# Kernel tuning notes

Measured on AMD Instinct MI355X. Metric: run time of the kernel, lower is better.

Reference implementation:

```python
import jax, jax.numpy as jnp
import numpy as np

B, T, RNN_DIM, ENC_DIM, ATT_DIM, NFILT, KSIZE = 256, 1024, 1024, 512, 128, 32, 31
PAD = (KSIZE - 1) // 2


def setup_inputs() -> dict:
    key = jax.random.key(0)
    ks = jax.random.split(key, 10)
    attn = jax.random.uniform(ks[3], (B, T), dtype=jnp.float32)
    attn = attn / jnp.sum(attn, axis=1, keepdims=True)  # previous-step alignment (sums to 1)
    return {
        "query": jax.random.normal(ks[0], (B, RNN_DIM), dtype=jnp.float32),
        "memory": jax.random.normal(ks[1], (B, T, ENC_DIM), dtype=jnp.float32),
        "processed_memory": jax.random.normal(ks[2], (B, T, ATT_DIM), dtype=jnp.float32),
        "attn_weights": attn,
        "attn_weights_cum": jax.random.uniform(ks[4], (B, T), dtype=jnp.float32),
        "memory_lengths": jax.random.randint(ks[5], (B,), T // 2, T + 1),
        "conv_w": jax.random.normal(ks[6], (NFILT, 2, KSIZE), dtype=jnp.float32) * 0.1,
        "W_loc": jax.random.normal(ks[7], (ATT_DIM, NFILT), dtype=jnp.float32) * 0.1,
        "W_q": jax.random.normal(ks[8], (ATT_DIM, RNN_DIM), dtype=jnp.float32) * 0.03,
        "v_w": jax.random.normal(ks[9], (1, ATT_DIM), dtype=jnp.float32) * 0.1,
        "v_b": jnp.zeros((1,), dtype=jnp.float32),
    }


def reference(query, memory, processed_memory, attn_weights, attn_weights_cum,
              memory_lengths, conv_w, W_loc, W_q, v_w, v_b):
    Tlen = memory.shape[1]
    # [B, 2, T]: stack prev + cumulative alignments
    cat = jnp.stack([attn_weights, attn_weights_cum], axis=1)
    # location conv: Conv1d(2 -> NFILT, k=31, same padding, no bias) -> [B, NFILT, T]
    loc = jax.lax.conv_general_dilated(
        cat, conv_w, window_strides=(1,), padding=[(PAD, PAD)],
        dimension_numbers=("NCH", "OIH", "NCH"))
    # location_dense: [B, T, ATT_DIM]
    processed_location = jnp.einsum("bct,ac->bta", loc, W_loc)
    # query projection: [B, 1, ATT_DIM]
    processed_query = (query @ W_q.T)[:, None, :]
    # additive energies: v . tanh(q + loc + mem) -> [B, T]
    hidden = jnp.tanh(processed_query + processed_location + processed_memory)
    energies = jnp.einsum("bta,a->bt", hidden, v_w[0]) + v_b[0]
    # mask padded positions (pos >= length) with -inf
    mask = jnp.arange(Tlen)[None, :] >= memory_lengths[:, None]
    energies = jnp.where(mask, -jnp.inf, energies)
    new_attn = jax.nn.softmax(energies, axis=1)
    new_cum = attn_weights_cum + new_attn
    # context: [B, ENC_DIM]
    context = jnp.einsum("bt,bte->be", new_attn, memory)
    return context, new_attn, new_cum
```

## Files before the change

kernel.cpp:

```cpp
#include <hip/hip_runtime.h>
#include <math.h>

#define Bc 256
#define Tc 1024
#define RNN_DIMc 1024
#define ENC_DIMc 512
#define ATT_DIMc 128
#define NFILTc 32
#define KSIZEc 31
#define PADc 15

__device__ __forceinline__ float fast_tanh(float x) {
    x = fminf(15.f, fmaxf(-15.f, x));
    float z = __expf(2.f * x);
    return (z - 1.f) / (z + 1.f);
}

__device__ __forceinline__ float wave_reduce_max(float x) {
#pragma unroll
    for (int off = 32; off > 0; off >>= 1) x = fmaxf(x, __shfl_xor(x, off, 64));
    return x;
}

__device__ __forceinline__ float wave_reduce_sum(float x) {
#pragma unroll
    for (int off = 32; off > 0; off >>= 1) x += __shfl_xor(x, off, 64);
    return x;
}

__global__ __launch_bounds__(128) void qproj_k(const float* __restrict__ query,
                                               const float* __restrict__ W_q,
                                               float* __restrict__ pq) {
    const int b = blockIdx.x;
    __shared__ float q[RNN_DIMc];
    for (int i = threadIdx.x; i < RNN_DIMc; i += 128) q[i] = query[b * RNN_DIMc + i];
    __syncthreads();
    const float* w = W_q + (size_t)threadIdx.x * RNN_DIMc;
    float acc = 0.f;
#pragma unroll 4
    for (int r = 0; r < RNN_DIMc; r += 4) {
        float4 wv = *(const float4*)(w + r);
        acc = fmaf(wv.x, q[r + 0], acc);
        acc = fmaf(wv.y, q[r + 1], acc);
        acc = fmaf(wv.z, q[r + 2], acc);
        acc = fmaf(wv.w, q[r + 3], acc);
    }
    pq[b * ATT_DIMc + threadIdx.x] = acc;
}

__global__ __launch_bounds__(256) void energies_k(
    const float* __restrict__ attn_w, const float* __restrict__ cum_w,
    const float* __restrict__ pm, const float* __restrict__ pq,
    const float* __restrict__ conv_w, const float* __restrict__ W_loc,
    const float* __restrict__ v_w, const float* __restrict__ v_b,
    const int* __restrict__ lens, float* __restrict__ energies) {
    const int b = blockIdx.x >> 2;
    const int t0 = (blockIdx.x & 3) * 256;
    const int t = t0 + threadIdx.x;

    __shared__ float s_a[256 + 2 * PADc];
    __shared__ float s_c[256 + 2 * PADc];
    for (int i = threadIdx.x; i < 256 + 2 * PADc; i += 256) {
        int tt = t0 - PADc + i;
        bool ok = (tt >= 0) && (tt < Tc);
        s_a[i] = ok ? attn_w[b * Tc + tt] : 0.f;
        s_c[i] = ok ? cum_w[b * Tc + tt] : 0.f;
    }
    __syncthreads();

    float wa[KSIZEc], wcm[KSIZEc];
#pragma unroll
    for (int k = 0; k < KSIZEc; ++k) {
        wa[k] = s_a[threadIdx.x + k];
        wcm[k] = s_c[threadIdx.x + k];
    }

    float loc[NFILTc];
#pragma unroll
    for (int f = 0; f < NFILTc; ++f) {
        const float* cw = conv_w + f * (2 * KSIZEc);
        float a0 = 0.f, a1 = 0.f;
#pragma unroll
        for (int k = 0; k < KSIZEc; ++k) {
            a0 = fmaf(cw[k], wa[k], a0);
            a1 = fmaf(cw[KSIZEc + k], wcm[k], a1);
        }
        loc[f] = a0 + a1;
    }

    const float* pmrow = pm + ((size_t)(b * Tc + t)) * ATT_DIMc;
    const float* pqr = pq + b * ATT_DIMc;
    float e = 0.f;
#pragma unroll 2
    for (int a = 0; a < ATT_DIMc; a += 4) {
        float4 pmv = *(const float4*)(pmrow + a);
        const float* wl = W_loc + a * NFILTc;
        float pl0 = 0.f, pl1 = 0.f, pl2 = 0.f, pl3 = 0.f;
#pragma unroll
        for (int f = 0; f < NFILTc; ++f) {
            float lf = loc[f];
            pl0 = fmaf(wl[f], lf, pl0);
            pl1 = fmaf(wl[NFILTc + f], lf, pl1);
            pl2 = fmaf(wl[2 * NFILTc + f], lf, pl2);
            pl3 = fmaf(wl[3 * NFILTc + f], lf, pl3);
        }
        e = fmaf(v_w[a + 0], fast_tanh(pqr[a + 0] + pl0 + pmv.x), e);
        e = fmaf(v_w[a + 1], fast_tanh(pqr[a + 1] + pl1 + pmv.y), e);
        e = fmaf(v_w[a + 2], fast_tanh(pqr[a + 2] + pl2 + pmv.z), e);
        e = fmaf(v_w[a + 3], fast_tanh(pqr[a + 3] + pl3 + pmv.w), e);
    }
    e += v_b[0];
    if (t >= lens[b]) e = -INFINITY;
    energies[b * Tc + t] = e;
}

__global__ __launch_bounds__(256) void softmax_k(const float* __restrict__ energies,
                                                 const float* __restrict__ cum_in,
                                                 float* __restrict__ out_attn,
                                                 float* __restrict__ out_cum) {
    const int b = blockIdx.x;
    const float* e = energies + b * Tc;
    float ev[4];
    float m = -INFINITY;
#pragma unroll
    for (int i = 0; i < 4; ++i) {
        ev[i] = e[threadIdx.x + 256 * i];
        m = fmaxf(m, ev[i]);
    }
    m = wave_reduce_max(m);
    __shared__ float redm[4];
    __shared__ float reds[4];
    const int wid = threadIdx.x >> 6;
    if ((threadIdx.x & 63) == 0) redm[wid] = m;
    __syncthreads();
    m = fmaxf(fmaxf(redm[0], redm[1]), fmaxf(redm[2], redm[3]));

    float p[4];
    float s = 0.f;
#pragma unroll
    for (int i = 0; i < 4; ++i) {
        p[i] = __expf(ev[i] - m);
        s += p[i];
    }
    s = wave_reduce_sum(s);
    if ((threadIdx.x & 63) == 0) reds[wid] = s;
    __syncthreads();
    s = reds[0] + reds[1] + reds[2] + reds[3];
    float inv = 1.f / s;
#pragma unroll
    for (int i = 0; i < 4; ++i) {
        int t = threadIdx.x + 256 * i;
        float na = p[i] * inv;
        out_attn[b * Tc + t] = na;
        out_cum[b * Tc + t] = cum_in[b * Tc + t] + na;
    }
}

__global__ __launch_bounds__(512) void ctx_partial_k(const float* __restrict__ attn,
                                                     const float* __restrict__ memory,
                                                     float* __restrict__ partial) {
    const int b = blockIdx.x >> 2;
    const int seg = blockIdx.x & 3;
    const int e = threadIdx.x;
    const float* ar = attn + b * Tc + seg * 256;
    const float* mr = memory + ((size_t)(b * Tc + seg * 256)) * ENC_DIMc + e;
    float acc = 0.f;
#pragma unroll 4
    for (int tt = 0; tt < 256; ++tt) {
        acc = fmaf(ar[tt], mr[(size_t)tt * ENC_DIMc], acc);
    }
    partial[(size_t)blockIdx.x * ENC_DIMc + e] = acc;
}

__global__ __launch_bounds__(256) void ctx_reduce_k(const float* __restrict__ partial,
                                                    float* __restrict__ ctx) {
    const int idx = blockIdx.x * 256 + threadIdx.x;
    const int b = idx >> 9;
    const int e = idx & 511;
    float s = partial[(size_t)(b * 4 + 0) * ENC_DIMc + e] +
              partial[(size_t)(b * 4 + 1) * ENC_DIMc + e] +
              partial[(size_t)(b * 4 + 2) * ENC_DIMc + e] +
              partial[(size_t)(b * 4 + 3) * ENC_DIMc + e];
    ctx[idx] = s;
}

extern "C" void kernel_launch(void* const* d_in, const int* in_sizes, int n_in,
                              void* d_out, int out_size, void* d_ws, size_t ws_size,
                              hipStream_t stream) {
    const float* query  = (const float*)d_in[0];
    const float* memory = (const float*)d_in[1];
    const float* pm     = (const float*)d_in[2];
    const float* attn_w = (const float*)d_in[3];
    const float* cum_w  = (const float*)d_in[4];
    const int*   lens   = (const int*)d_in[5];
    const float* conv_w = (const float*)d_in[6];
    const float* W_loc  = (const float*)d_in[7];
    const float* W_q    = (const float*)d_in[8];
    const float* v_w    = (const float*)d_in[9];
    const float* v_b    = (const float*)d_in[10];

    float* out      = (float*)d_out;
    float* ctx      = out;
    float* out_attn = out + Bc * ENC_DIMc;
    float* out_cum  = out + Bc * ENC_DIMc + Bc * Tc;

    float* pq       = (float*)d_ws;
    float* energies = pq + Bc * ATT_DIMc;
    float* partial  = (float*)d_ws;

    qproj_k<<<Bc, 128, 0, stream>>>(query, W_q, pq);
    energies_k<<<Bc * 4, 256, 0, stream>>>(attn_w, cum_w, pm, pq, conv_w, W_loc, v_w, v_b,
                                           lens, energies);
    softmax_k<<<Bc, 256, 0, stream>>>(energies, cum_w, out_attn, out_cum);
    ctx_partial_k<<<Bc * 4, 512, 0, stream>>>(out_attn, memory, partial);
    ctx_reduce_k<<<(Bc * ENC_DIMc) / 256, 256, 0, stream>>>(partial, ctx);
}
```

Before: 861.2 us.

## Fuse all attention stages into one per-batch 1024-thread kernel

```diff
diff --git a/kernel.cpp b/kernel.cpp
--- a/kernel.cpp
+++ b/kernel.cpp
@@ -28,160 +28,144 @@
     return x;
 }
 
-__global__ __launch_bounds__(128) void qproj_k(const float* __restrict__ query,
-                                               const float* __restrict__ W_q,
-                                               float* __restrict__ pq) {
+__global__ __launch_bounds__(1024) void lsa_fused(
+    const float* __restrict__ query, const float* __restrict__ memory,
+    const float* __restrict__ pm, const float* __restrict__ attn_w,
+    const float* __restrict__ cum_w, const int* __restrict__ lens,
+    const float* __restrict__ conv_w, const float* __restrict__ W_loc,
+    const float* __restrict__ W_q, const float* __restrict__ v_w,
+    const float* __restrict__ v_b, float* __restrict__ ctx,
+    float* __restrict__ out_attn, float* __restrict__ out_cum) {
     const int b = blockIdx.x;
-    __shared__ float q[RNN_DIMc];
-    for (int i = threadIdx.x; i < RNN_DIMc; i += 128) q[i] = query[b * RNN_DIMc + i];
-    __syncthreads();
-    const float* w = W_q + (size_t)threadIdx.x * RNN_DIMc;
-    float acc = 0.f;
-#pragma unroll 4
-    for (int r = 0; r < RNN_DIMc; r += 4) {
-        float4 wv = *(const float4*)(w + r);
-        acc = fmaf(wv.x, q[r + 0], acc);
-        acc = fmaf(wv.y, q[r + 1], acc);
-        acc = fmaf(wv.z, q[r + 2], acc);
-        acc = fmaf(wv.w, q[r + 3], acc);
-    }
-    pq[b * ATT_DIMc + threadIdx.x] = acc;
-}
+    const int tid = threadIdx.x;
 
-__global__ __launch_bounds__(256) void energies_k(
-    const float* __restrict__ attn_w, const float* __restrict__ cum_w,
-    const float* __restrict__ pm, const float* __restrict__ pq,
-    const float* __restrict__ conv_w, const float* __restrict__ W_loc,
-    const float* __restrict__ v_w, const float* __restrict__ v_b,
-    const int* __restrict__ lens, float* __restrict__ energies) {
-    const int b = blockIdx.x >> 2;
-    const int t0 = (blockIdx.x & 3) * 256;
-    const int t = t0 + threadIdx.x;
+    __shared__ float s_q[RNN_DIMc];
+    __shared__ float s_pq[ATT_DIMc];
+    __shared__ float s_win0[Tc + 2 * PADc];
+    __shared__ float s_win1[Tc + 2 * PADc];
+    __shared__ float s_attn[Tc];
+    __shared__ float s_redm[16];
+    __shared__ float s_reds[16];
+    __shared__ float s_scratch[8][ENC_DIMc];
 
-    __shared__ float s_a[256 + 2 * PADc];
-    __shared__ float s_c[256 + 2 * PADc];
-    for (int i = threadIdx.x; i < 256 + 2 * PADc; i += 256) {
-        int tt = t0 - PADc + i;
+    if (tid < RNN_DIMc) s_q[tid] = query[b * RNN_DIMc + tid];
+    for (int i = tid; i < Tc + 2 * PADc; i += 1024) {
+        int tt = i - PADc;
         bool ok = (tt >= 0) && (tt < Tc);
-        s_a[i] = ok ? attn_w[b * Tc + tt] : 0.f;
-        s_c[i] = ok ? cum_w[b * Tc + tt] : 0.f;
+        s_win0[i] = ok ? attn_w[b * Tc + tt] : 0.f;
+        s_win1[i] = ok ? cum_w[b * Tc + tt] : 0.f;
     }
     __syncthreads();
 
-    float wa[KSIZEc], wcm[KSIZEc];
+    {
+        const int a = tid >> 3;
+        const int c = tid & 7;
+        const float* w = W_q + (size_t)a * RNN_DIMc + c * 128;
+        const float* qq = s_q + c * 128;
+        float acc = 0.f;
 #pragma unroll
-    for (int k = 0; k < KSIZEc; ++k) {
-        wa[k] = s_a[threadIdx.x + k];
-        wcm[k] = s_c[threadIdx.x + k];
+        for (int j = 0; j < 128; j += 4) {
+            float4 wv = *(const float4*)(w + j);
+            acc = fmaf(wv.x, qq[j + 0], acc);
+            acc = fmaf(wv.y, qq[j + 1], acc);
+            acc = fmaf(wv.z, qq[j + 2], acc);
+            acc = fmaf(wv.w, qq[j + 3], acc);
+        }
+        ((float*)s_scratch)[a * 8 + c] = acc;
+    }
+    __syncthreads();
+    if (tid < ATT_DIMc) {
+        const float* p = (const float*)s_scratch + tid * 8;
+        s_pq[tid] = p[0] + p[1] + p[2] + p[3] + p[4] + p[5] + p[6] + p[7];
+    }
+    __syncthreads();
+
+    const int t = tid;
+    float e;
+    {
+        float loc[NFILTc];
+#pragma unroll
+        for (int f = 0; f < NFILTc; ++f) loc[f] = 0.f;
+        for (int k = 0; k < KSIZEc; ++k) {
+            const float wa = s_win0[t + k];
+            const float wc = s_win1[t + k];
+#pragma unroll
+            for (int f = 0; f < NFILTc; ++f) {
+                loc[f] = fmaf(conv_w[f * (2 * KSIZEc) + k], wa, loc[f]);
+                loc[f] = fmaf(conv_w[f * (2 * KSIZEc) + KSIZEc + k], wc, loc[f]);
+            }
+        }
+
+        const float* pmrow = pm + ((size_t)(b * Tc + t)) * ATT_DIMc;
+        e = 0.f;
+#pragma unroll 2
+        for (int a = 0; a < ATT_DIMc; a += 4) {
+            float4 pmv = *(const float4*)(pmrow + a);
+            const float* wl = W_loc + a * NFILTc;
+            float pl0 = 0.f, pl1 = 0.f, pl2 = 0.f, pl3 = 0.f;
+#pragma unroll
+            for (int f = 0; f < NFILTc; ++f) {
+                float lf = loc[f];
+                pl0 = fmaf(wl[f], lf, pl0);
+                pl1 = fmaf(wl[NFILTc + f], lf, pl1);
+                pl2 = fmaf(wl[2 * NFILTc + f], lf, pl2);
+                pl3 = fmaf(wl[3 * NFILTc + f], lf, pl3);
+            }
+            e = fmaf(v_w[a + 0], fast_tanh(s_pq[a + 0] + pl0 + pmv.x), e);
+            e = fmaf(v_w[a + 1], fast_tanh(s_pq[a + 1] + pl1 + pmv.y), e);
+            e = fmaf(v_w[a + 2], fast_tanh(s_pq[a + 2] + pl2 + pmv.z), e);
+            e = fmaf(v_w[a + 3], fast_tanh(s_pq[a + 3] + pl3 + pmv.w), e);
+        }
+        e += v_b[0];
+        if (t >= lens[b]) e = -INFINITY;
     }
 
-    float loc[NFILTc];
+    {
+        float m = wave_reduce_max(e);
+        if ((tid & 63) == 0) s_redm[tid >> 6] = m;
+        __syncthreads();
+        float bm = s_redm[0];
 #pragma unroll
-    for (int f = 0; f < NFILTc; ++f) {
-        const float* cw = conv_w + f * (2 * KSIZEc);
-        float a0 = 0.f, a1 = 0.f;
+        for (int j = 1; j < 16; ++j) bm = fmaxf(bm, s_redm[j]);
+
+        float p = __expf(e - bm);
+        float s = wave_reduce_sum(p);
+        if ((tid & 63) == 0) s_reds[tid >> 6] = s;
+        __syncthreads();
+        float tot = 0.f;
 #pragma unroll
-        for (int k = 0; k < KSIZEc; ++k) {
-            a0 = fmaf(cw[k], wa[k], a0);
-            a1 = fmaf(cw[KSIZEc + k], wcm[k], a1);
+        for (int j = 0; j < 16; ++j) tot += s_reds[j];
+        float na = p * (1.f / tot);
+
+        out_attn[b * Tc + t] = na;
+        out_cum[b * Tc + t] = s_win1[t + PADc] + na;
+        s_attn[t] = na;
+    }
+    __syncthreads();
+
+    {
+        const int tr = tid >> 7;
+        const int e4 = (tid & 127) * 4;
+        const float* mb = memory + (size_t)b * Tc * ENC_DIMc;
+        float4 acc = make_float4(0.f, 0.f, 0.f, 0.f);
+#pragma unroll 4
+        for (int tt = tr; tt < Tc; tt += 8) {
+            const float w = s_attn[tt];
+            const float4 mv = *(const float4*)(mb + (size_t)tt * ENC_DIMc + e4);
+            acc.x = fmaf(w, mv.x, acc.x);
+            acc.y = fmaf(w, mv.y, acc.y);
+            acc.z = fmaf(w, mv.z, acc.z);
+            acc.w = fmaf(w, mv.w, acc.w);
         }
-        loc[f] = a0 + a1;
+        *(float4*)&s_scratch[tr][e4] = acc;
     }
-
-    const float* pmrow = pm + ((size_t)(b * Tc + t)) * ATT_DIMc;
-    const float* pqr = pq + b * ATT_DIMc;
-    float e = 0.f;
-#pragma unroll 2
-    for (int a = 0; a < ATT_DIMc; a += 4) {
-        float4 pmv = *(const float4*)(pmrow + a);
-        const float* wl = W_loc + a * NFILTc;
-        float pl0 = 0.f, pl1 = 0.f, pl2 = 0.f, pl3 = 0.f;
+    __syncthreads();
+    if (tid < ENC_DIMc) {
+        float s = 0.f;
 #pragma unroll
-        for (int f = 0; f < NFILTc; ++f) {
-            float lf = loc[f];
-            pl0 = fmaf(wl[f], lf, pl0);
-            pl1 = fmaf(wl[NFILTc + f], lf, pl1);
-            pl2 = fmaf(wl[2 * NFILTc + f], lf, pl2);
-            pl3 = fmaf(wl[3 * NFILTc + f], lf, pl3);
-        }
-        e = fmaf(v_w[a + 0], fast_tanh(pqr[a + 0] + pl0 + pmv.x), e);
-        e = fmaf(v_w[a + 1], fast_tanh(pqr[a + 1] + pl1 + pmv.y), e);
-        e = fmaf(v_w[a + 2], fast_tanh(pqr[a + 2] + pl2 + pmv.z), e);
-        e = fmaf(v_w[a + 3], fast_tanh(pqr[a + 3] + pl3 + pmv.w), e);
+        for (int j = 0; j < 8; ++j) s += s_scratch[j][tid];
+        ctx[b * ENC_DIMc + tid] = s;
     }
-    e += v_b[0];
-    if (t >= lens[b]) e = -INFINITY;
-    energies[b * Tc + t] = e;
-}
-
-__global__ __launch_bounds__(256) void softmax_k(const float* __restrict__ energies,
-                                                 const float* __restrict__ cum_in,
-                                                 float* __restrict__ out_attn,
-                                                 float* __restrict__ out_cum) {
-    const int b = blockIdx.x;
-    const float* e = energies + b * Tc;
-    float ev[4];
-    float m = -INFINITY;
-#pragma unroll
-    for (int i = 0; i < 4; ++i) {
-        ev[i] = e[threadIdx.x + 256 * i];
-        m = fmaxf(m, ev[i]);
-    }
-    m = wave_reduce_max(m);
-    __shared__ float redm[4];
-    __shared__ float reds[4];
-    const int wid = threadIdx.x >> 6;
-    if ((threadIdx.x & 63) == 0) redm[wid] = m;
-    __syncthreads();
-    m = fmaxf(fmaxf(redm[0], redm[1]), fmaxf(redm[2], redm[3]));
-
-    float p[4];
-    float s = 0.f;
-#pragma unroll
-    for (int i = 0; i < 4; ++i) {
-        p[i] = __expf(ev[i] - m);
-        s += p[i];
-    }
-    s = wave_reduce_sum(s);
-    if ((threadIdx.x & 63) == 0) reds[wid] = s;
-    __syncthreads();
-    s = reds[0] + reds[1] + reds[2] + reds[3];
-    float inv = 1.f / s;
-#pragma unroll
-    for (int i = 0; i < 4; ++i) {
-        int t = threadIdx.x + 256 * i;
-        float na = p[i] * inv;
-        out_attn[b * Tc + t] = na;
-        out_cum[b * Tc + t] = cum_in[b * Tc + t] + na;
-    }
-}
-
-__global__ __launch_bounds__(512) void ctx_partial_k(const float* __restrict__ attn,
-                                                     const float* __restrict__ memory,
-                                                     float* __restrict__ partial) {
-    const int b = blockIdx.x >> 2;
-    const int seg = blockIdx.x & 3;
-    const int e = threadIdx.x;
-    const float* ar = attn + b * Tc + seg * 256;
-    const float* mr = memory + ((size_t)(b * Tc + seg * 256)) * ENC_DIMc + e;
-    float acc = 0.f;
-#pragma unroll 4
-    for (int tt = 0; tt < 256; ++tt) {
-        acc = fmaf(ar[tt], mr[(size_t)tt * ENC_DIMc], acc);
-    }
-    partial[(size_t)blockIdx.x * ENC_DIMc + e] = acc;
-}
-
-__global__ __launch_bounds__(256) void ctx_reduce_k(const float* __restrict__ partial,
-                                                    float* __restrict__ ctx) {
-    const int idx = blockIdx.x * 256 + threadIdx.x;
-    const int b = idx >> 9;
-    const int e = idx & 511;
-    float s = partial[(size_t)(b * 4 + 0) * ENC_DIMc + e] +
-              partial[(size_t)(b * 4 + 1) * ENC_DIMc + e] +
-              partial[(size_t)(b * 4 + 2) * ENC_DIMc + e] +
-              partial[(size_t)(b * 4 + 3) * ENC_DIMc + e];
-    ctx[idx] = s;
 }
 
 extern "C" void kernel_launch(void* const* d_in, const int* in_sizes, int n_in,
@@ -204,14 +188,7 @@
     float* out_attn = out + Bc * ENC_DIMc;
     float* out_cum  = out + Bc * ENC_DIMc + Bc * Tc;
 
-    float* pq       = (float*)d_ws;
-    float* energies = pq + Bc * ATT_DIMc;
-    float* partial  = (float*)d_ws;
-
-    qproj_k<<<Bc, 128, 0, stream>>>(query, W_q, pq);
-    energies_k<<<Bc * 4, 256, 0, stream>>>(attn_w, cum_w, pm, pq, conv_w, W_loc, v_w, v_b,
-                                           lens, energies);
-    softmax_k<<<Bc, 256, 0, stream>>>(energies, cum_w, out_attn, out_cum);
-    ctx_partial_k<<<Bc * 4, 512, 0, stream>>>(out_attn, memory, partial);
-    ctx_reduce_k<<<(Bc * ENC_DIMc) / 256, 256, 0, stream>>>(partial, ctx);
+    lsa_fused<<<Bc, 1024, 0, stream>>>(query, memory, pm, attn_w, cum_w, lens,
+                                       conv_w, W_loc, W_q, v_w, v_b,
+                                       ctx, out_attn, out_cum);
 }
```

Result: faster. 829.2 us (-3.7%).
